# Performance work log

Measured on AMD Instinct MI355X. Metric: run time of the kernel, lower is better.

## Reference

```python
import jax, jax.numpy as jnp
import numpy as np

B, T, D, H, O = 256, 512, 128, 256, 128

def setup_inputs() -> dict:
    key = jax.random.key(0)
    ks = jax.random.split(key, 7)
    s = lambda k, shape, fan: jax.random.normal(k, shape, dtype=jnp.float32) / np.sqrt(fan)
    return {
        "x": jax.random.normal(ks[0], (B, T, D), dtype=jnp.float32),
        "W_hx_w": s(ks[1], (H, D), D),
        "W_hx_b": jnp.zeros((H,), jnp.float32),
        "W_hh_w": s(ks[2], (H, H), H),
        "W_hh_b": jnp.zeros((H,), jnp.float32),
        "W_ph_w": s(ks[3], (O, H), H),
        "W_ph_b": jnp.zeros((O,), jnp.float32),
    }

def reference(x, W_hx_w, W_hx_b, W_hh_w, W_hh_b, W_ph_w, W_ph_b):
    # Precompute the input projection for all timesteps in one batched GEMM.
    xW = jnp.einsum('btd,hd->bth', x, W_hx_w) + W_hx_b  # [B,T,H]
    h0 = jnp.zeros((x.shape[0], W_hh_w.shape[0]), x.dtype)

    def step(h, xw_t):
        h_new = jnp.tanh(xw_t + h @ W_hh_w.T + W_hh_b)
        return h_new, None

    h_T, _ = jax.lax.scan(step, h0, jnp.swapaxes(xW, 0, 1))  # scan over T
    out = h_T @ W_ph_w.T + W_ph_b  # [B,O]
    return out
```

## Files before the change

kernel.cpp:

```cpp
#include <hip/hip_runtime.h>


typedef _Float16 f16;
typedef _Float16 f16x2 __attribute__((ext_vector_type(2)));
typedef _Float16 f16x4 __attribute__((ext_vector_type(4)));
typedef _Float16 f16x8 __attribute__((ext_vector_type(8)));
typedef float f32x4 __attribute__((ext_vector_type(4)));

#define NB 256
#define NT 512
#define ND 128
#define NH 256
#define NO 128
#define R  16
#define TCH 8
#define NCH (NT / TCH)
#define STEP_F16 4096
#define WS_NEED ((size_t)16 * NT * STEP_F16 * 2)

__device__ __forceinline__ float fast_tanh(float z) {
  float e = __builtin_amdgcn_exp2f(z * 2.88539008177793f);
  float r = __builtin_amdgcn_rcpf(e + 1.0f);
  return __builtin_fmaf(-2.0f, r, 1.0f);
}

__device__ __forceinline__ f16x8 cvt8(const float* __restrict__ p) {
  f32x4 v0 = *(const f32x4*)p;
  f32x4 v1 = *(const f32x4*)(p + 4);
  f16x8 r;
  r[0] = (f16)v0.x; r[1] = (f16)v0.y; r[2] = (f16)v0.z; r[3] = (f16)v0.w;
  r[4] = (f16)v1.x; r[5] = (f16)v1.y; r[6] = (f16)v1.z; r[7] = (f16)v1.w;
  return r;
}

__device__ __forceinline__ f16x8 cvt44(const float* __restrict__ p0,
                                       const float* __restrict__ p1) {
  f32x4 a = *(const f32x4*)p0;
  f32x4 b = *(const f32x4*)p1;
  f16x8 r;
  r[0] = (f16)a.x; r[1] = (f16)a.y; r[2] = (f16)a.z; r[3] = (f16)a.w;
  r[4] = (f16)b.x; r[5] = (f16)b.y; r[6] = (f16)b.z; r[7] = (f16)b.w;
  return r;
}

__global__ __launch_bounds__(256, 1)
void xw_gemm(const float* __restrict__ x,
             const float* __restrict__ Wx, const float* __restrict__ bx,
             const float* __restrict__ bh, f16* __restrict__ ws)
{
  const int bid = blockIdx.x;
  const int wgb = bid & 15;
  const int c0  = (bid >> 4) * 4;
  const int tid = threadIdx.x;
  const int w   = tid >> 6;
  const int l15 = tid & 15;
  const int g   = (tid >> 4) & 3;

  __shared__ alignas(16) f16 xlds[TCH * R][ND];

  f16x8 fWx[4][4];
  f32x4 bias4[4];
  #pragma unroll
  for (int ct = 0; ct < 4; ++ct) {
    const int j = w * 64 + ct * 16 + l15;
    #pragma unroll
    for (int kt = 0; kt < 4; ++kt)
      fWx[ct][kt] = cvt8(Wx + (size_t)j * ND + kt * 32 + g * 8);
    const int j0 = w * 64 + ct * 16 + g * 4;
    #pragma unroll
    for (int rg = 0; rg < 4; ++rg)
      bias4[ct][rg] = bx[j0 + rg] + bh[j0 + rg];
  }

  const int srow = tid >> 4;
  const int sq   = tid & 15;

  #pragma unroll 1
  for (int it = 0; it < 4; ++it) {
    const int c = c0 + it;
    if (it) __syncthreads();

    const float* xc = x + ((size_t)(wgb * R + srow) * NT + (size_t)c * TCH) * ND;
    #pragma unroll
    for (int jj = 0; jj < 16; ++jj) {
      const int f = (sq + jj * 16) * 4;
      f32x4 v = *(const f32x4*)(xc + f);
      const int t = f >> 7;
      const int d = f & (ND - 1);
      const int m = t * R + srow;
      f16x4 h4;
      h4[0] = (f16)v.x; h4[1] = (f16)v.y; h4[2] = (f16)v.z; h4[3] = (f16)v.w;
      *(f16x4*)((char*)&xlds[m][0] + ((2 * d) ^ ((m & 7) << 4))) = h4;
    }
    __syncthreads();

    #pragma unroll
    for (int t = 0; t < TCH; ++t) {
      f16x8 b[4];
      #pragma unroll
      for (int kt = 0; kt < 4; ++kt) {
        const int m = t * R + l15;
        b[kt] = *(const f16x8*)((char*)&xlds[m][0] +
                 ((kt * 64 + g * 16) ^ ((m & 7) << 4)));
      }
      f16* wsp = ws + ((size_t)(wgb * NT + c * TCH + t)) * STEP_F16
                    + w * 1024 + g * 64 + l15 * 4;
      #pragma unroll
      for (int ct = 0; ct < 4; ++ct) {
        f32x4 ac = bias4[ct];
        #pragma unroll
        for (int kt = 0; kt < 4; ++kt)
          ac = __builtin_amdgcn_mfma_f32_16x16x32_f16(fWx[ct][kt], b[kt], ac, 0, 0, 0);
        f16x4 p;
        p[0] = (f16)ac[0]; p[1] = (f16)ac[1]; p[2] = (f16)ac[2]; p[3] = (f16)ac[3];
        *(f16x4*)(wsp + ct * 256) = p;
      }
    }
  }
}

#define DO_STEP(CUR, ACIN, ACOUT, XWPF, XWIN, TAU)                          \
  {                                                                         \
    f16x8 bfr[8];                                                           \
    _Pragma("unroll")                                                       \
    for (int kt = 0; kt < 8; ++kt)                                          \
      bfr[kt] = *(const f16x8*)((const char*)&hbuf[CUR][l15][0] +           \
                (((kt * 4 + g + l15) & 31) << 4));                          \
    int pf = (TAU) + 2; pf = pf < NT ? pf : NT - 1;                         \
    _Pragma("unroll")                                                       \
    for (int ct = 0; ct < 2; ++ct)                                          \
      XWPF[ct] = *(const f16x4*)(wsg + (size_t)pf * STEP_F16 + ct * 256);   \
    _Pragma("unroll")                                                       \
    for (int ct = 0; ct < 2; ++ct) {                                        \
      _Pragma("unroll")                                                     \
      for (int kt = 0; kt < 8; ++kt)                                        \
        ACIN[ct] = __builtin_amdgcn_mfma_f32_16x16x32_f16(fWh[ct][kt],      \
                     bfr[kt], ACIN[ct], 0, 0, 0);                           \
    }                                                                       \
    {                                                                       \
      f16x8 h8;                                                             \
      _Pragma("unroll")                                                     \
      for (int ct = 0; ct < 2; ++ct)                                        \
        _Pragma("unroll")                                                   \
        for (int rg = 0; rg < 4; ++rg)                                      \
          h8[ct * 4 + rg] = (f16)fast_tanh(ACIN[ct][rg]);                   \
      *(f16x8*)((char*)&hbuf[(CUR) ^ 1][l15][0] +                           \
                (((w2 * 4 + g + l15) & 31) << 4)) = h8;                     \
    }                                                                       \
    _Pragma("unroll")                                                       \
    for (int ct = 0; ct < 2; ++ct) {                                        \
      ACOUT[ct][0] = (float)XWIN[ct][0]; ACOUT[ct][1] = (float)XWIN[ct][1]; \
      ACOUT[ct][2] = (float)XWIN[ct][2]; ACOUT[ct][3] = (float)XWIN[ct][3]; \
    }                                                                       \
    asm volatile("s_waitcnt lgkmcnt(0)\n\ts_barrier" ::: "memory");         \
    __builtin_amdgcn_sched_barrier(0);                                      \
  }

__global__ __launch_bounds__(512, 2)
void rnn_scan(const f16* __restrict__ ws,
              const float* __restrict__ Wh,
              const float* __restrict__ Wp, const float* __restrict__ bp,
              float* __restrict__ out)
{
  const int wg  = blockIdx.x;
  const int tid = threadIdx.x;
  const int w2  = tid >> 6;
  const int l15 = tid & 15;
  const int g   = (tid >> 4) & 3;

  __shared__ alignas(16) f16 hbuf[2][R][NH];

  f16x8 fWh[2][8];
  #pragma unroll
  for (int ct = 0; ct < 2; ++ct) {
    const int j = w2 * 32 + ct * 16 + l15;
    #pragma unroll
    for (int kt = 0; kt < 8; ++kt)
      fWh[ct][kt] = cvt44(Wh + (size_t)j * NH + kt * 32 + g * 4,
                          Wh + (size_t)j * NH + kt * 32 + 16 + g * 4);
  }

  {
    unsigned* hz = (unsigned*)&hbuf[0][0][0];
    #pragma unroll
    for (int k = 0; k < (2 * R * NH / 2) / 512; ++k) hz[tid + k * 512] = 0u;
  }

  const f16* wsg = ws + (size_t)wg * NT * STEP_F16
                 + (size_t)(w2 * 2) * 256 + g * 64 + l15 * 4;

  f16x4 xA[2], xB[2];
  #pragma unroll
  for (int ct = 0; ct < 2; ++ct) xA[ct] = *(const f16x4*)(wsg + 0 * STEP_F16 + ct * 256);
  #pragma unroll
  for (int ct = 0; ct < 2; ++ct) xB[ct] = *(const f16x4*)(wsg + 1 * STEP_F16 + ct * 256);

  f32x4 acA[2], acB[2];
  #pragma unroll
  for (int ct = 0; ct < 2; ++ct) {
    acA[ct][0] = (float)xA[ct][0]; acA[ct][1] = (float)xA[ct][1];
    acA[ct][2] = (float)xA[ct][2]; acA[ct][3] = (float)xA[ct][3];
  }
  __syncthreads();

  #pragma unroll 1
  for (int tau = 0; tau < NT; tau += 2) {
    DO_STEP(0, acA, acB, xA, xB, tau);
    DO_STEP(1, acB, acA, xB, xA, tau + 1);
  }

  f16x8 bh8[8];
  #pragma unroll
  for (int kt = 0; kt < 8; ++kt)
    bh8[kt] = *(const f16x8*)((const char*)&hbuf[0][l15][0] +
              (((kt * 4 + g + l15) & 31) << 4));
  {
    const int j0 = w2 * 16 + g * 4;
    f32x4 ac = {bp[j0], bp[j0 + 1], bp[j0 + 2], bp[j0 + 3]};
    #pragma unroll
    for (int kt = 0; kt < 8; ++kt) {
      const float* wrow = Wp + (size_t)(w2 * 16 + l15) * NH;
      f16x8 afr = cvt44(wrow + kt * 32 + g * 4, wrow + kt * 32 + 16 + g * 4);
      ac = __builtin_amdgcn_mfma_f32_16x16x32_f16(afr, bh8[kt], ac, 0, 0, 0);
    }
    #pragma unroll
    for (int rg = 0; rg < 4; ++rg)
      out[(size_t)(wg * R + l15) * NO + j0 + rg] = ac[rg];
  }
}

__global__ __launch_bounds__(256, 1)
void rnn_mfma(const float* __restrict__ x,
              const float* __restrict__ Wx, const float* __restrict__ bx,
              const float* __restrict__ Wh, const float* __restrict__ bh,
              const float* __restrict__ Wp, const float* __restrict__ bp,
              float* __restrict__ out)
{
  const int wg  = blockIdx.x;
  const int tid = threadIdx.x;
  const int w   = tid >> 6;
  const int l15 = tid & 15;
  const int g   = (tid >> 4) & 3;

  __shared__ alignas(16) f16 xlds[TCH * R][ND];
  __shared__ alignas(16) f16 hbuf[2][R][NH];

  f16x8 fWh[4][8];
  #pragma unroll
  for (int ct = 0; ct < 4; ++ct) {
    const int j = w * 64 + ct * 16 + l15;
    #pragma unroll
    for (int kt = 0; kt < 8; ++kt)
      fWh[ct][kt] = cvt8(Wh + (size_t)j * NH + kt * 32 + g * 8);
  }
  f16x8 fWx[4][4];
  #pragma unroll
  for (int ct = 0; ct < 4; ++ct) {
    const int j = w * 64 + ct * 16 + l15;
    #pragma unroll
    for (int kt = 0; kt < 4; ++kt)
      fWx[ct][kt] = cvt8(Wx + (size_t)j * ND + kt * 32 + g * 8);
  }
  float bias[4];
  #pragma unroll
  for (int ct = 0; ct < 4; ++ct) {
    const int j = w * 64 + ct * 16 + l15;
    bias[ct] = bx[j] + bh[j];
  }
  {
    unsigned* hz = (unsigned*)&hbuf[0][0][0];
    #pragma unroll
    for (int k = 0; k < (R * NH / 2) / 256; ++k) hz[tid + k * 256] = 0u;
  }
  __syncthreads();

  int cur = 0;
  f16x2 xwb[TCH][4][2];
  const int srow = tid >> 4;
  const int sq   = tid & 15;
  const float* xrow = x + (size_t)(wg * R + srow) * NT * ND;

  #pragma unroll 1
  for (int c = 0; c < NCH; ++c) {
    const float* xc = xrow + (size_t)c * TCH * ND;
    #pragma unroll
    for (int jj = 0; jj < 16; ++jj) {
      const int f = (sq + jj * 16) * 4;
      f32x4 v = *(const f32x4*)(xc + f);
      const int t = f >> 7;
      const int d = f & (ND - 1);
      const int m = t * R + srow;
      f16x4 h4;
      h4[0] = (f16)v.x; h4[1] = (f16)v.y; h4[2] = (f16)v.z; h4[3] = (f16)v.w;
      *(f16x4*)((char*)&xlds[m][0] + ((2 * d) ^ ((m & 7) << 4))) = h4;
    }
    __syncthreads();

    #pragma unroll
    for (int t = 0; t < TCH; ++t) {
      f16x8 a[4];
      #pragma unroll
      for (int kt = 0; kt < 4; ++kt) {
        const int m = t * R + l15;
        a[kt] = *(const f16x8*)((char*)&xlds[m][0] +
                 ((kt * 64 + g * 16) ^ ((m & 7) << 4)));
      }
      #pragma unroll
      for (int ct = 0; ct < 4; ++ct) {
        f32x4 ac = {bias[ct], bias[ct], bias[ct], bias[ct]};
        #pragma unroll
        for (int kt = 0; kt < 4; ++kt)
          ac = __builtin_amdgcn_mfma_f32_16x16x32_f16(a[kt], fWx[ct][kt], ac, 0, 0, 0);
        f16x2 p0; p0[0] = (f16)ac[0]; p0[1] = (f16)ac[1];
        f16x2 p1; p1[0] = (f16)ac[2]; p1[1] = (f16)ac[3];
        xwb[t][ct][0] = p0;
        xwb[t][ct][1] = p1;
      }
    }

    #pragma unroll
    for (int s = 0; s < TCH; ++s) {
      f16x8 a[8];
      #pragma unroll
      for (int kt = 0; kt < 8; ++kt) {
        const int m = l15;
        a[kt] = *(const f16x8*)((char*)&hbuf[cur][m][0] +
                 ((kt * 64 + g * 16) ^ ((m & 7) << 4)));
      }
      const int nxt = cur ^ 1;
      #pragma unroll
      for (int ct = 0; ct < 4; ++ct) {
        f32x4 ac  = {(float)xwb[s][ct][0][0], (float)xwb[s][ct][0][1],
                     (float)xwb[s][ct][1][0], (float)xwb[s][ct][1][1]};
        f32x4 ac2 = {0.f, 0.f, 0.f, 0.f};
        #pragma unroll
        for (int kt = 0; kt < 4; ++kt) {
          ac  = __builtin_amdgcn_mfma_f32_16x16x32_f16(a[2*kt],     fWh[ct][2*kt],     ac,  0, 0, 0);
          ac2 = __builtin_amdgcn_mfma_f32_16x16x32_f16(a[2*kt + 1], fWh[ct][2*kt + 1], ac2, 0, 0, 0);
        }
        #pragma unroll
        for (int rg = 0; rg < 4; ++rg) {
          const float th = fast_tanh(ac[rg] + ac2[rg]);
          const int row = g * 4 + rg;
          const int col = w * 64 + ct * 16 + l15;
          *(f16*)((char*)&hbuf[nxt][row][0] +
                  ((2 * col) ^ ((row & 7) << 4))) = (f16)th;
        }
      }
      cur = nxt;
      __syncthreads();
    }
  }

  f16x8 ah[8];
  #pragma unroll
  for (int kt = 0; kt < 8; ++kt) {
    const int m = l15;
    ah[kt] = *(const f16x8*)((char*)&hbuf[cur][m][0] +
             ((kt * 64 + g * 16) ^ ((m & 7) << 4)));
  }
  #pragma unroll
  for (int ct = 0; ct < 2; ++ct) {
    const int o = w * 32 + ct * 16 + l15;
    f32x4 ac = {bp[o], bp[o], bp[o], bp[o]};
    #pragma unroll
    for (int kt = 0; kt < 8; ++kt) {
      f16x8 bfr = cvt8(Wp + (size_t)o * NH + kt * 32 + g * 8);
      ac = __builtin_amdgcn_mfma_f32_16x16x32_f16(ah[kt], bfr, ac, 0, 0, 0);
    }
    #pragma unroll
    for (int rg = 0; rg < 4; ++rg) {
      const int row = g * 4 + rg;
      out[(size_t)(wg * R + row) * NO + o] = ac[rg];
    }
  }
}

extern "C" void kernel_launch(void* const* d_in, const int* in_sizes, int n_in,
                              void* d_out, int out_size, void* d_ws, size_t ws_size,
                              hipStream_t stream) {
  const float* x   = (const float*)d_in[0];
  const float* whx = (const float*)d_in[1];
  const float* bhx = (const float*)d_in[2];
  const float* whh = (const float*)d_in[3];
  const float* bhh = (const float*)d_in[4];
  const float* wph = (const float*)d_in[5];
  const float* bph = (const float*)d_in[6];
  float* out = (float*)d_out;

  if (ws_size >= WS_NEED) {
    f16* ws = (f16*)d_ws;
    xw_gemm<<<dim3(256), dim3(256), 0, stream>>>(x, whx, bhx, bhh, ws);
    rnn_scan<<<dim3(16), dim3(512), 0, stream>>>(ws, whh, wph, bph, out);
  } else {
    rnn_mfma<<<dim3(NB / R), dim3(256), 0, stream>>>(x, whx, bhx, whh, bhh, wph, bph, out);
  }
}
```

Measured before the change: 339.7 us.

## Keep own h slice in registers and rotate K order in recurrent scan

In the recurrent scan, each wave keeps the h chunk it just produced in registers and rotates its K-tile order so that chunk is consumed first. This skips one LDS read per step and lets the first MFMAs start before the other waves' chunks are read. The W_hh fragments are loaded in the matching rotated order. Separately, the input-projection GEMM now launches one block per time chunk (1024 blocks, two per CU) instead of looping four chunks per block, which trades fewer reused weight loads for more parallelism.

```diff
diff --git a/kernel.cpp b/kernel.cpp
--- a/kernel.cpp
+++ b/kernel.cpp
@@ -43,14 +43,13 @@
   return r;
 }
 
-__global__ __launch_bounds__(256, 1)
+__global__ __launch_bounds__(256, 2)
 void xw_gemm(const float* __restrict__ x,
              const float* __restrict__ Wx, const float* __restrict__ bx,
              const float* __restrict__ bh, f16* __restrict__ ws)
 {
-  const int bid = blockIdx.x;
-  const int wgb = bid & 15;
-  const int c0  = (bid >> 4) * 4;
+  const int wgb = blockIdx.x & 15;
+  const int c   = blockIdx.x >> 4;
   const int tid = threadIdx.x;
   const int w   = tid >> 6;
   const int l15 = tid & 15;
@@ -74,68 +73,65 @@
 
   const int srow = tid >> 4;
   const int sq   = tid & 15;
-
-  #pragma unroll 1
-  for (int it = 0; it < 4; ++it) {
-    const int c = c0 + it;
-    if (it) __syncthreads();
-
-    const float* xc = x + ((size_t)(wgb * R + srow) * NT + (size_t)c * TCH) * ND;
-    #pragma unroll
-    for (int jj = 0; jj < 16; ++jj) {
-      const int f = (sq + jj * 16) * 4;
-      f32x4 v = *(const f32x4*)(xc + f);
-      const int t = f >> 7;
-      const int d = f & (ND - 1);
-      const int m = t * R + srow;
-      f16x4 h4;
-      h4[0] = (f16)v.x; h4[1] = (f16)v.y; h4[2] = (f16)v.z; h4[3] = (f16)v.w;
-      *(f16x4*)((char*)&xlds[m][0] + ((2 * d) ^ ((m & 7) << 4))) = h4;
-    }
-    __syncthreads();
-
-    #pragma unroll
-    for (int t = 0; t < TCH; ++t) {
-      f16x8 b[4];
+  const float* xc = x + ((size_t)(wgb * R + srow) * NT + (size_t)c * TCH) * ND;
+  #pragma unroll
+  for (int jj = 0; jj < 16; ++jj) {
+    const int f = (sq + jj * 16) * 4;
+    f32x4 v = *(const f32x4*)(xc + f);
+    const int t = f >> 7;
+    const int d = f & (ND - 1);
+    const int m = t * R + srow;
+    f16x4 h4;
+    h4[0] = (f16)v.x; h4[1] = (f16)v.y; h4[2] = (f16)v.z; h4[3] = (f16)v.w;
+    *(f16x4*)((char*)&xlds[m][0] + ((2 * d) ^ ((m & 7) << 4))) = h4;
+  }
+  __syncthreads();
+
+  #pragma unroll
+  for (int t = 0; t < TCH; ++t) {
+    f16x8 b[4];
+    #pragma unroll
+    for (int kt = 0; kt < 4; ++kt) {
+      const int m = t * R + l15;
+      b[kt] = *(const f16x8*)((char*)&xlds[m][0] +
+               ((kt * 64 + g * 16) ^ ((m & 7) << 4)));
+    }
+    f16* wsp = ws + ((size_t)(wgb * NT + c * TCH + t)) * STEP_F16
+                  + w * 1024 + g * 64 + l15 * 4;
+    #pragma unroll
+    for (int ct = 0; ct < 4; ++ct) {
+      f32x4 ac = bias4[ct];
       #pragma unroll
-      for (int kt = 0; kt < 4; ++kt) {
-        const int m = t * R + l15;
-        b[kt] = *(const f16x8*)((char*)&xlds[m][0] +
-                 ((kt * 64 + g * 16) ^ ((m & 7) << 4)));
-      }
-      f16* wsp = ws + ((size_t)(wgb * NT + c * TCH + t)) * STEP_F16
-                    + w * 1024 + g * 64 + l15 * 4;
-      #pragma unroll
-      for (int ct = 0; ct < 4; ++ct) {
-        f32x4 ac = bias4[ct];
-        #pragma unroll
-        for (int kt = 0; kt < 4; ++kt)
-          ac = __builtin_amdgcn_mfma_f32_16x16x32_f16(fWx[ct][kt], b[kt], ac, 0, 0, 0);
-        f16x4 p;
-        p[0] = (f16)ac[0]; p[1] = (f16)ac[1]; p[2] = (f16)ac[2]; p[3] = (f16)ac[3];
-        *(f16x4*)(wsp + ct * 256) = p;
-      }
-    }
-  }
-}
-
-#define DO_STEP(CUR, ACIN, ACOUT, XWPF, XWIN, TAU)                          \
+      for (int kt = 0; kt < 4; ++kt)
+        ac = __builtin_amdgcn_mfma_f32_16x16x32_f16(fWx[ct][kt], b[kt], ac, 0, 0, 0);
+      f16x4 p;
+      p[0] = (f16)ac[0]; p[1] = (f16)ac[1]; p[2] = (f16)ac[2]; p[3] = (f16)ac[3];
+      *(f16x4*)(wsp + ct * 256) = p;
+    }
+  }
+}
+
+#define DO_STEP(CUR, ACIN, ACOUT, XWPF, XWIN, H8K, TAU)                     \
   {                                                                         \
-    f16x8 bfr[8];                                                           \
+    f16x8 bfr[7];                                                           \
     _Pragma("unroll")                                                       \
-    for (int kt = 0; kt < 8; ++kt)                                          \
-      bfr[kt] = *(const f16x8*)((const char*)&hbuf[CUR][l15][0] +           \
-                (((kt * 4 + g + l15) & 31) << 4));                          \
+    for (int kr = 1; kr < 8; ++kr)                                          \
+      bfr[kr - 1] = *(const f16x8*)((const char*)&hbuf[CUR][l15][0] +       \
+                ((((w2 + kr) * 4 + g + l15) & 31) << 4));                   \
     int pf = (TAU) + 2; pf = pf < NT ? pf : NT - 1;                         \
     _Pragma("unroll")                                                       \
     for (int ct = 0; ct < 2; ++ct)                                          \
       XWPF[ct] = *(const f16x4*)(wsg + (size_t)pf * STEP_F16 + ct * 256);   \
     _Pragma("unroll")                                                       \
-    for (int ct = 0; ct < 2; ++ct) {                                        \
+    for (int ct = 0; ct < 2; ++ct)                                          \
+      ACIN[ct] = __builtin_amdgcn_mfma_f32_16x16x32_f16(fWh[ct][0], H8K,    \
+                   ACIN[ct], 0, 0, 0);                                      \
+    _Pragma("unroll")                                                       \
+    for (int kr = 1; kr < 8; ++kr) {                                        \
       _Pragma("unroll")                                                     \
-      for (int kt = 0; kt < 8; ++kt)                                        \
-        ACIN[ct] = __builtin_amdgcn_mfma_f32_16x16x32_f16(fWh[ct][kt],      \
-                     bfr[kt], ACIN[ct], 0, 0, 0);                           \
+      for (int ct = 0; ct < 2; ++ct)                                        \
+        ACIN[ct] = __builtin_amdgcn_mfma_f32_16x16x32_f16(fWh[ct][kr],      \
+                     bfr[kr - 1], ACIN[ct], 0, 0, 0);                       \
     }                                                                       \
     {                                                                       \
       f16x8 h8;                                                             \
@@ -146,6 +142,7 @@
           h8[ct * 4 + rg] = (f16)fast_tanh(ACIN[ct][rg]);                   \
       *(f16x8*)((char*)&hbuf[(CUR) ^ 1][l15][0] +                           \
                 (((w2 * 4 + g + l15) & 31) << 4)) = h8;                     \
+      H8K = h8;                                                             \
     }                                                                       \
     _Pragma("unroll")                                                       \
     for (int ct = 0; ct < 2; ++ct) {                                        \
@@ -175,9 +172,11 @@
   for (int ct = 0; ct < 2; ++ct) {
     const int j = w2 * 32 + ct * 16 + l15;
     #pragma unroll
-    for (int kt = 0; kt < 8; ++kt)
-      fWh[ct][kt] = cvt44(Wh + (size_t)j * NH + kt * 32 + g * 4,
-                          Wh + (size_t)j * NH + kt * 32 + 16 + g * 4);
+    for (int kr = 0; kr < 8; ++kr) {
+      const int kta = (w2 + kr) & 7;
+      fWh[ct][kr] = cvt44(Wh + (size_t)j * NH + kta * 32 + g * 4,
+                          Wh + (size_t)j * NH + kta * 32 + 16 + g * 4);
+    }
   }
 
   {
@@ -201,12 +200,17 @@
     acA[ct][0] = (float)xA[ct][0]; acA[ct][1] = (float)xA[ct][1];
     acA[ct][2] = (float)xA[ct][2]; acA[ct][3] = (float)xA[ct][3];
   }
+
+  f16x8 h8k;
+  #pragma unroll
+  for (int i = 0; i < 8; ++i) h8k[i] = (f16)0.f;
+
   __syncthreads();
 
   #pragma unroll 1
   for (int tau = 0; tau < NT; tau += 2) {
-    DO_STEP(0, acA, acB, xA, xB, tau);
-    DO_STEP(1, acB, acA, xB, xA, tau + 1);
+    DO_STEP(0, acA, acB, xA, xB, h8k, tau);
+    DO_STEP(1, acB, acA, xB, xA, h8k, tau + 1);
   }
 
   f16x8 bh8[8];
@@ -390,7 +394,7 @@
 
   if (ws_size >= WS_NEED) {
     f16* ws = (f16*)d_ws;
-    xw_gemm<<<dim3(256), dim3(256), 0, stream>>>(x, whx, bhx, bhh, ws);
+    xw_gemm<<<dim3(16 * NCH), dim3(256), 0, stream>>>(x, whx, bhx, bhh, ws);
     rnn_scan<<<dim3(16), dim3(512), 0, stream>>>(ws, whh, wph, bph, out);
   } else {
     rnn_mfma<<<dim3(NB / R), dim3(256), 0, stream>>>(x, whx, bhx, whh, bhh, wph, bph, out);
```

New measurement: 330.2 us. 2.8% less time.
